# Optimization experiments

Measured on AMD Instinct MI355X. Metric: run time of the kernel, lower is better.

## Reference

```python
import jax, jax.numpy as jnp
import numpy as np

N, F, H, EMB, R, E, B = 100000, 128, 128, 64, 3, 1600000, 1024


def rgcn_conv(x, edge_src, edge_dst, edge_type, W_rel, W_root, b):
    # PyG RGCNConv with aggr='mean': out_i = x_i @ W_root + b + sum_r mean_{j in N_r(i)} x_j @ W_r
    n = x.shape[0]
    r = W_rel.shape[0]
    xr = jnp.einsum('nf,rfh->rnh', x, W_rel)            # [R,N,H] per-relation transform
    msg = xr[edge_type, edge_src]                       # [E,H] gather per edge
    seg = edge_type.astype(jnp.int32) * n + edge_dst    # fused (rel, dst) segment id
    agg = jax.ops.segment_sum(msg, seg, num_segments=r * n).reshape(r, n, -1)
    cnt = jax.ops.segment_sum(jnp.ones((msg.shape[0],), msg.dtype), seg, num_segments=r * n)
    cnt = cnt.reshape(r, n, 1)
    agg = agg / jnp.maximum(cnt, 1.0)
    return agg.sum(0) + x @ W_root + b


def setup_inputs() -> dict:
    key = jax.random.key(0)
    ks = jax.random.split(key, 16)
    s = 0.05
    return {
        'x': jax.random.normal(ks[0], (N, F), jnp.float32),
        'edge_src': jax.random.randint(ks[1], (E,), 0, N, jnp.int32),
        'edge_dst': jax.random.randint(ks[2], (E,), 0, N, jnp.int32),
        'edge_type': jax.random.randint(ks[3], (E,), 0, R, jnp.int32),
        'edge_attr': jax.random.uniform(ks[4], (E, 2), jnp.float32),
        'nest': jax.random.randint(ks[5], (B,), 0, N, jnp.int32),
        'food': jax.random.randint(ks[6], (B,), 0, N, jnp.int32),
        'W_rel1': jax.random.normal(ks[7], (R, F, H), jnp.float32) * s,
        'W_root1': jax.random.normal(ks[8], (F, H), jnp.float32) * s,
        'b1': jnp.zeros((H,), jnp.float32),
        'W_rel2': jax.random.normal(ks[9], (R, H, EMB), jnp.float32) * s,
        'W_root2': jax.random.normal(ks[10], (H, EMB), jnp.float32) * s,
        'b2': jnp.zeros((EMB,), jnp.float32),
        'fc_W': jax.random.normal(ks[11], (2 * EMB, H), jnp.float32) * s,
        'fc_b': jnp.zeros((H,), jnp.float32),
    }


def reference(x, edge_src, edge_dst, edge_type, edge_attr, nest, food,
              W_rel1, W_root1, b1, W_rel2, W_root2, b2, fc_W, fc_b):
    # distance binning (computed in the original forward but unused downstream)
    d = edge_attr[:, 0]
    dmin, dmax = d.min(), d.max()
    bin_size = (dmax - dmin) / 3
    binned = jnp.clip(jnp.floor((d - dmin) / bin_size), 0, 2)
    del binned

    h1 = jax.nn.relu(rgcn_conv(x, edge_src, edge_dst, edge_type, W_rel1, W_root1, b1))
    node = rgcn_conv(h1, edge_src, edge_dst, edge_type, W_rel2, W_root2, b2)  # [N,EMB]
    pair = jnp.concatenate([node[nest], node[food]], axis=-1)  # [B, 2*EMB]
    return jnp.tanh(pair @ fc_W + fc_b)
```

## Files before the change

kernel.cpp:

```cpp
#include <hip/hip_runtime.h>
#include <stdint.h>

typedef unsigned short u16;
typedef __attribute__((ext_vector_type(8))) short short8;
typedef __attribute__((ext_vector_type(4))) float f32x4;
typedef __attribute__((ext_vector_type(2))) float f32x2;
typedef __attribute__((ext_vector_type(4))) unsigned int u32x4;

#define N_NODES 100000
#define RREL    3
#define NEDGE   1600000
#define NPAIR   1024
#define NSEG    (RREL * N_NODES)

#define EPB   4096
#define NBLK  ((NEDGE + EPB - 1) / EPB)
#define DPB   512
#define NBIN  ((N_NODES + DPB - 1) / DPB)
#define LSEG  (DPB * RREL)
#define CAP   12288

#define PREP_TW   384
#define PREP_CAST (N_NODES * 128 / 4 / 256)

__device__ __forceinline__ float bflo(unsigned int u) {
    union { unsigned int u; float f; } c; c.u = u << 16; return c.f;
}
__device__ __forceinline__ float bfhi(unsigned int u) {
    union { unsigned int u; float f; } c; c.u = u & 0xffff0000u; return c.f;
}
__device__ __forceinline__ u16 f2bf(float f) {
    union { float f; unsigned int u; } c; c.f = f;
    unsigned int u = c.u;
    u += 0x7fffu + ((u >> 16) & 1u);
    return (u16)(u >> 16);
}

__device__ __forceinline__ void async_copy16(const u16* g, u16* l) {
    __builtin_amdgcn_global_load_lds(
        (const __attribute__((address_space(1))) unsigned int*)g,
        (__attribute__((address_space(3))) unsigned int*)l,
        16, 0, 0);
}

__global__ __launch_bounds__(256) void prep_kernel(const int* __restrict__ es,
                                                   const int* __restrict__ ed,
                                                   const int* __restrict__ et,
                                                   int* __restrict__ gpos,
                                                   unsigned int* __restrict__ binned,
                                                   const float* __restrict__ x,
                                                   u16* __restrict__ xb,
                                                   const float* __restrict__ Wrel1,
                                                   const float* __restrict__ Wroot1,
                                                   const float* __restrict__ Wrel2,
                                                   const float* __restrict__ Wroot2,
                                                   u16* __restrict__ Wt1,
                                                   u16* __restrict__ Wt2) {
    __shared__ int h[NBIN];
    __shared__ int base[NBIN];
    int b = blockIdx.x, t = threadIdx.x;
    if (b < NBLK) {
        for (int i = t; i < NBIN; i += 256) h[i] = 0;
        __syncthreads();
        int e0 = b * EPB;
        int e1 = e0 + EPB; if (e1 > NEDGE) e1 = NEDGE;
        for (int i = e0 + t; i < e1; i += 256)
            atomicAdd(&h[ed[i] >> 9], 1);
        __syncthreads();
        for (int i = t; i < NBIN; i += 256) {
            int c = h[i];
            base[i] = c ? atomicAdd(&gpos[i], c) : 0;
            h[i] = 0;
        }
        __syncthreads();
        for (int i = e0 + t; i < e1; i += 256) {
            int d = ed[i];
            int bin = d >> 9;
            unsigned int pk = ((unsigned int)es[i] << 11) | (unsigned int)((d & 511) * 3 + et[i]);
            int off = atomicAdd(&h[bin], 1);
            binned[(size_t)bin * CAP + base[bin] + off] = pk;
        }
    } else if (b < NBLK + PREP_TW) {
        int idx = (b - NBLK) * 256 + t;
        if (idx < 128 * 512) {
            int n = idx >> 9, k = idx & 511;
            float v = (k < 384) ? Wrel1[(size_t)k * 128 + n] : Wroot1[(size_t)(k - 384) * 128 + n];
            Wt1[idx] = f2bf(v);
        } else {
            int j = idx - 128 * 512;
            if (j < 256 * 128) {
                int n = j >> 7, k = j & 127;
                float v = (n < 192) ? Wrel2[((size_t)(n >> 6) * 128 + k) * 64 + (n & 63)]
                                    : Wroot2[(size_t)k * 64 + (n - 192)];
                Wt2[j] = f2bf(v);
            }
        }
    } else {
        int i = (b - NBLK - PREP_TW) * 256 + t;
        f32x4 v = __builtin_nontemporal_load(&((const f32x4*)x)[i]);
        uint2 o;
        o.x = ((unsigned int)f2bf(v.y) << 16) | (unsigned int)f2bf(v.x);
        o.y = ((unsigned int)f2bf(v.w) << 16) | (unsigned int)f2bf(v.z);
        ((uint2*)xb)[i] = o;
    }
}

__global__ __launch_bounds__(256) void p4_finalize(const unsigned int* __restrict__ binned,
                                                   const int* __restrict__ gpos,
                                                   int* __restrict__ seg_start,
                                                   int* __restrict__ cnt,
                                                   int* __restrict__ sorted_src) {
    __shared__ int h[LSEG];
    __shared__ int cur[LSEG];
    __shared__ int wtot4[4];
    int t = threadIdx.x, bin = blockIdx.x;
    for (int i = t; i < LSEG; i += 256) h[i] = 0;
    __syncthreads();
    int eb = bin * CAP;
    int ee = eb + gpos[bin];
    for (int i = eb + t; i < ee; i += 256)
        atomicAdd(&h[binned[i] & 2047u], 1);
    __syncthreads();
    int i6 = t * 6;
    int s = 0;
    #pragma unroll
    for (int i = 0; i < 6; ++i) s += h[i6 + i];
    int lane = t & 63, wv = t >> 6;
    int incl = s;
    #pragma unroll
    for (int d = 1; d < 64; d <<= 1) { int v = __shfl_up(incl, d); if (lane >= d) incl += v; }
    if (lane == 63) wtot4[wv] = incl;
    __syncthreads();
    int wpre = 0;
    #pragma unroll
    for (int i = 0; i < 4; ++i) if (i < wv) wpre += wtot4[i];
    int run = wpre + incl - s;
    int segbase = bin * LSEG;
    #pragma unroll
    for (int i = 0; i < 6; ++i) {
        int ls = i6 + i;
        int c = h[ls];
        int seg = segbase + ls;
        if (seg < NSEG) { seg_start[seg] = eb + run; cnt[seg] = c; }
        cur[ls] = run;
        run += c;
    }
    __syncthreads();
    for (int i = eb + t; i < ee; i += 256) {
        unsigned int u = binned[i];
        int ls = (int)(u & 2047u);
        int p = atomicAdd(&cur[ls], 1);
        sorted_src[eb + p] = (int)(u >> 11);
    }
}

__global__ __launch_bounds__(512, 8) void fused_l1(const uint4* __restrict__ X4,
                                                   const u16* __restrict__ xb,
                                                   const int* __restrict__ seg_start,
                                                   const int* __restrict__ cnt,
                                                   const int* __restrict__ sorted_src,
                                                   const u16* __restrict__ Wt1,
                                                   const float* __restrict__ b1,
                                                   u16* __restrict__ h1) {
    __shared__ __align__(16) u16 Aagg[32 * 392];
    __shared__ __align__(16) u16 Aroot[32 * 32];
    __shared__ __align__(16) u16 Bs[128 * 32];
    const int t = threadIdx.x;
    const int w = t >> 6, l = t & 63;
    const int q4 = l >> 4, ql = l & 15;
    const int qid = w * 4 + q4;
    const int bm  = blockIdx.x * 32;
    const int bm3 = blockIdx.x * 96;
    const int shbase = q4 * 16;

    int cArr[3], stArr[3];
    #pragma unroll
    for (int sp = 0; sp < 3; ++sp) {
        int wid = bm3 + sp * 32 + qid;
        cArr[sp]  = cnt[wid];
        stArr[sp] = seg_start[wid];
    }
    #pragma unroll 1
    for (int sp = 0; sp < 3; ++sp) {
        int seg_local = sp * 32 + qid;
        int c  = cArr[sp];
        int st = stArr[sp];

        float a0 = 0.f, a1 = 0.f, a2 = 0.f, a3 = 0.f,
              a4 = 0.f, a5 = 0.f, a6 = 0.f, a7 = 0.f;

        for (int base = 0; base < c; base += 16) {
            int rem = c - base;
            int ii  = (ql < rem) ? ql : (rem - 1);
            int idxv = sorted_src[st + base + ii];
            int lim = (rem < 16) ? rem : 16;
            for (int j = 0; j < lim; j += 4) {
                int e1 = j + 1, e2 = j + 2, e3 = j + 3;
                float w1 = (e1 < lim) ? 1.f : 0.f;
                float w2 = (e2 < lim) ? 1.f : 0.f;
                float w3 = (e3 < lim) ? 1.f : 0.f;
                int s0 = __shfl(idxv, shbase + j);
                int s1 = __shfl(idxv, shbase + ((e1 < lim) ? e1 : 0));
                int s2 = __shfl(idxv, shbase + ((e2 < lim) ? e2 : 0));
                int s3 = __shfl(idxv, shbase + ((e3 < lim) ? e3 : 0));
                uint4 v0 = X4[(size_t)s0 * 16 + ql];
                uint4 v1 = X4[(size_t)s1 * 16 + ql];
                uint4 v2 = X4[(size_t)s2 * 16 + ql];
                uint4 v3 = X4[(size_t)s3 * 16 + ql];
                a0 += bflo(v0.x);               a1 += bfhi(v0.x);
                a2 += bflo(v0.y);               a3 += bfhi(v0.y);
                a4 += bflo(v0.z);               a5 += bfhi(v0.z);
                a6 += bflo(v0.w);               a7 += bfhi(v0.w);
                a0 = fmaf(w1, bflo(v1.x), a0);  a1 = fmaf(w1, bfhi(v1.x), a1);
                a2 = fmaf(w1, bflo(v1.y), a2);  a3 = fmaf(w1, bfhi(v1.y), a3);
                a4 = fmaf(w1, bflo(v1.z), a4);  a5 = fmaf(w1, bfhi(v1.z), a5);
                a6 = fmaf(w1, bflo(v1.w), a6);  a7 = fmaf(w1, bfhi(v1.w), a7);
                a0 = fmaf(w2, bflo(v2.x), a0);  a1 = fmaf(w2, bfhi(v2.x), a1);
                a2 = fmaf(w2, bflo(v2.y), a2);  a3 = fmaf(w2, bfhi(v2.y), a3);
                a4 = fmaf(w2, bflo(v2.z), a4);  a5 = fmaf(w2, bfhi(v2.z), a5);
                a6 = fmaf(w2, bflo(v2.w), a6);  a7 = fmaf(w2, bfhi(v2.w), a7);
                a0 = fmaf(w3, bflo(v3.x), a0);  a1 = fmaf(w3, bfhi(v3.x), a1);
                a2 = fmaf(w3, bflo(v3.y), a2);  a3 = fmaf(w3, bfhi(v3.y), a3);
                a4 = fmaf(w3, bflo(v3.z), a4);  a5 = fmaf(w3, bfhi(v3.z), a5);
                a6 = fmaf(w3, bflo(v3.w), a6);  a7 = fmaf(w3, bfhi(v3.w), a7);
            }
        }
        float sc = 1.0f / (float)(c > 0 ? c : 1);
        u32x4 o;
        o.x = ((unsigned int)f2bf(a1 * sc) << 16) | (unsigned int)f2bf(a0 * sc);
        o.y = ((unsigned int)f2bf(a3 * sc) << 16) | (unsigned int)f2bf(a2 * sc);
        o.z = ((unsigned int)f2bf(a5 * sc) << 16) | (unsigned int)f2bf(a4 * sc);
        o.w = ((unsigned int)f2bf(a7 * sc) << 16) | (unsigned int)f2bf(a6 * sc);
        int n_loc = seg_local / 3;
        int rel   = seg_local - n_loc * 3;
        *(u32x4*)&Aagg[n_loc * 392 + rel * 128 + ql * 8] = o;
    }
    __syncthreads();

    const int wm = w >> 2, wn = w & 3;
    const int q = l >> 4, lm = l & 15;
    f32x4 acc[2] = {};
    const int br  = t >> 2;
    const int bc4 = (t & 3) * 8;

    for (int kt = 0; kt < 16; ++kt) {
        const int k0 = kt * 32;
        __syncthreads();
        async_copy16(Wt1 + (size_t)br * 512 + k0 + bc4, &Bs[br * 32 + bc4]);
        if (kt >= 12 && w < 2) {
            async_copy16(xb + (size_t)(bm + br) * 128 + (k0 - 384) + bc4, &Aroot[br * 32 + bc4]);
        }
        __syncthreads();
        short8 fa;
        if (kt < 12) fa = *(const short8*)&Aagg[(wm * 16 + lm) * 392 + k0 + q * 8];
        else         fa = *(const short8*)&Aroot[(wm * 16 + lm) * 32 + q * 8];
        #pragma unroll
        for (int ni = 0; ni < 2; ++ni) {
            short8 fb = *(const short8*)&Bs[(wn * 32 + ni * 16 + lm) * 32 + q * 8];
            acc[ni] = __builtin_amdgcn_mfma_f32_16x16x32_bf16(fa, fb, acc[ni], 0, 0, 0);
        }
    }
    #pragma unroll
    for (int ni = 0; ni < 2; ++ni) {
        int gc = wn * 32 + ni * 16 + lm;
        float bv = b1[gc];
        #pragma unroll
        for (int rg = 0; rg < 4; ++rg) {
            int gr = bm + wm * 16 + q * 4 + rg;
            float v = fmaxf(acc[ni][rg] + bv, 0.0f);
            h1[(size_t)gr * 128 + gc] = f2bf(v);
        }
    }
}

__global__ __launch_bounds__(256) void seg_pair(const u16* __restrict__ P,
                                                const int* __restrict__ seg_start,
                                                const int* __restrict__ cnt,
                                                const int* __restrict__ sorted_src,
                                                const float* __restrict__ node,
                                                const int* __restrict__ nest,
                                                const int* __restrict__ food,
                                                float* __restrict__ pairbuf) {
    int lane = threadIdx.x & 63;
    int q4 = lane >> 4, ql = lane & 15;
    int e  = ql >> 3;
    int fl = ql & 7;
    int slot = ((blockIdx.x * 256 + threadIdx.x) >> 6) * 4 + q4;
    int p = slot >> 1, side = slot & 1;
    int dst = side ? food[p] : nest[p];
    if ((unsigned)dst >= (unsigned)N_NODES) dst = 0;
    int shbase = q4 * 16;

    int c0 = cnt[dst * 3 + 0], c1 = cnt[dst * 3 + 1], c2 = cnt[dst * 3 + 2];
    int st = seg_start[dst * 3 + 0];
    int c01 = c0 + c1, tot = c01 + c2;
    float r0 = c0 ? 1.0f / (float)c0 : 0.0f;
    float r1 = c1 ? 1.0f / (float)c1 : 0.0f;
    float r2 = c2 ? 1.0f / (float)c2 : 0.0f;

    const f32x4* np = (const f32x4*)(node + (size_t)dst * 64 + fl * 8);
    f32x4 z0 = *np;
    f32x4 z1 = *(np + 1);

    f32x2 d0 = {0.f,0.f}, d1 = {0.f,0.f}, d2 = {0.f,0.f}, d3 = {0.f,0.f};

    for (int base = 0; base < tot; base += 16) {
        int rem = tot - base;
        int ii  = (ql < rem) ? ql : 0;
        int idxv = sorted_src[st + base + ii];
        int lim = (rem < 16) ? rem : 16;

        uint4 v[8];
        #pragma unroll
        for (int k = 0; k < 8; ++k) {
            int jj = 2 * k + e;
            int sel = (jj < lim) ? jj : 0;
            int s = __shfl(idxv, shbase + sel);
            int ge = base + sel;
            int rel = (ge >= c0) + (ge >= c01);
            v[k] = *(const uint4*)(P + (size_t)s * 192 + rel * 64 + fl * 8);
        }
        #pragma unroll
        for (int k = 0; k < 8; ++k) {
            int jj = 2 * k + e;
            int ge = base + jj;
            float wr = (jj < lim) ? ((ge < c0) ? r0 : ((ge < c01) ? r1 : r2)) : 0.0f;
            f32x2 wv = {wr, wr};
            d0 += wv * (f32x2){bflo(v[k].x), bfhi(v[k].x)};
            d1 += wv * (f32x2){bflo(v[k].y), bfhi(v[k].y)};
            d2 += wv * (f32x2){bflo(v[k].z), bfhi(v[k].z)};
            d3 += wv * (f32x2){bflo(v[k].w), bfhi(v[k].w)};
        }
    }
    d0.x += __shfl_xor(d0.x, 8); d0.y += __shfl_xor(d0.y, 8);
    d1.x += __shfl_xor(d1.x, 8); d1.y += __shfl_xor(d1.y, 8);
    d2.x += __shfl_xor(d2.x, 8); d2.y += __shfl_xor(d2.y, 8);
    d3.x += __shfl_xor(d3.x, 8); d3.y += __shfl_xor(d3.y, 8);
    if (e == 0) {
        f32x4 o0 = {z0.x + d0.x, z0.y + d0.y, z0.z + d1.x, z0.w + d1.y};
        f32x4 o1 = {z1.x + d2.x, z1.y + d2.y, z1.z + d3.x, z1.w + d3.y};
        f32x4* op = (f32x4*)(pairbuf + (size_t)p * 128 + side * 64 + fl * 8);
        *op       = o0;
        *(op + 1) = o1;
    }
}

template <int BM, int BN, int KTOT, int KLO, bool RELU, int OMODE>
__global__ __launch_bounds__(256) void gemm_fused(const u16* __restrict__ Alo,
                                                  const u16* __restrict__ Ahi,
                                                  const u16* __restrict__ Wt,
                                                  const float* __restrict__ bias,
                                                  void* __restrict__ OutV,
                                                  float* __restrict__ Out2) {
    constexpr int M = N_NODES;
    constexpr int BK = 32;
    __shared__ __align__(16) u16 As[BM * BK];
    __shared__ __align__(16) u16 Bs[BN * BK];
    const int t = threadIdx.x;
    const int w = t >> 6, l = t & 63;
    const int bm = blockIdx.x * BM;
    constexpr int WN  = BN / 64;
    constexpr int WM  = 4 / WN;
    constexpr int WTM = BM / WM;
    constexpr int WTN = 64;
    constexpr int MI = WTM / 16, NI = WTN / 16;
    const int wm = w / WN, wn = w % WN;
    const int q = l >> 4, lm = l & 15;

    f32x4 acc[MI][NI] = {};

    const int ar = t >> 2;
    const int ac = (t & 3) * 8;

    int gr0 = bm + ar;       if (gr0 >= M) gr0 = M - 1;
    int gr1 = bm + 64 + ar;  if (gr1 >= M) gr1 = M - 1;

    for (int kt = 0; kt < KTOT / BK; ++kt) {
        const int k0 = kt * BK;
        const u16* base; int stride, kk;
        if (k0 < KLO) { base = Alo; stride = KLO == KTOT ? KTOT : 384; kk = k0; }
        else          { base = Ahi; stride = 128; kk = k0 - KLO; }
        __syncthreads();
        async_copy16(base + (size_t)gr0 * stride + kk + ac, &As[ar * BK + ac]);
        if (BM == 128)
            async_copy16(base + (size_t)gr1 * stride + kk + ac, &As[(64 + ar) * BK + ac]);
        #pragma unroll
        for (int i = 0; i < BN / 64; ++i)
            async_copy16(Wt + (size_t)(i * 64 + ar) * KTOT + k0 + ac,
                         &Bs[(i * 64 + ar) * BK + ac]);
        __syncthreads();
        short8 fa[MI], fb[NI];
        #pragma unroll
        for (int mi = 0; mi < MI; ++mi)
            fa[mi] = *(const short8*)&As[(wm * WTM + mi * 16 + lm) * BK + q * 8];
        #pragma unroll
        for (int ni = 0; ni < NI; ++ni)
            fb[ni] = *(const short8*)&Bs[(wn * WTN + ni * 16 + lm) * BK + q * 8];
        #pragma unroll
        for (int mi = 0; mi < MI; ++mi)
            #pragma unroll
            for (int ni = 0; ni < NI; ++ni)
                acc[mi][ni] = __builtin_amdgcn_mfma_f32_16x16x32_bf16(
                    fa[mi], fb[ni], acc[mi][ni], 0, 0, 0);
    }
    #pragma unroll
    for (int mi = 0; mi < MI; ++mi) {
        #pragma unroll
        for (int ni = 0; ni < NI; ++ni) {
            int gc = wn * WTN + ni * 16 + lm;
            float bv;
            if (OMODE == 2) bv = (gc >= 192) ? bias[gc - 192] : 0.0f;
            else            bv = bias[gc];
            #pragma unroll
            for (int rg = 0; rg < 4; ++rg) {
                int gr = bm + wm * WTM + mi * 16 + q * 4 + rg;
                if (gr < M) {
                    float v = acc[mi][ni][rg] + bv;
                    if (RELU) v = fmaxf(v, 0.0f);
                    if (OMODE == 0)      ((u16*)OutV)[(size_t)gr * BN + gc] = f2bf(v);
                    else if (OMODE == 1) ((float*)OutV)[(size_t)gr * BN + gc] = v;
                    else {
                        if (gc < 192) ((u16*)OutV)[(size_t)gr * 192 + gc] = f2bf(v);
                        else          Out2[(size_t)gr * 64 + (gc - 192)] = v;
                    }
                }
            }
        }
    }
}

__global__ __launch_bounds__(128) void pair_mlp(const float* __restrict__ pairbuf,
                                                const float* __restrict__ fcW,
                                                const float* __restrict__ fcb,
                                                float* __restrict__ out) {
    int p = blockIdx.x;
    int t = threadIdx.x;
    __shared__ float pv[128];
    pv[t] = pairbuf[(size_t)p * 128 + t];
    __syncthreads();
    float s = fcb[t];
    #pragma unroll 4
    for (int k = 0; k < 128; ++k)
        s += pv[k] * fcW[k * 128 + t];
    out[(size_t)p * 128 + t] = tanhf(s);
}

extern "C" void kernel_launch(void* const* d_in, const int* in_sizes, int n_in,
                              void* d_out, int out_size, void* d_ws, size_t ws_size,
                              hipStream_t stream) {
    const float* x    = (const float*)d_in[0];
    const int* esrc   = (const int*)d_in[1];
    const int* edst   = (const int*)d_in[2];
    const int* etyp   = (const int*)d_in[3];
    const int* nest   = (const int*)d_in[5];
    const int* food   = (const int*)d_in[6];
    const float* Wrel1  = (const float*)d_in[7];
    const float* Wroot1 = (const float*)d_in[8];
    const float* b1     = (const float*)d_in[9];
    const float* Wrel2  = (const float*)d_in[10];
    const float* Wroot2 = (const float*)d_in[11];
    const float* b2     = (const float*)d_in[12];
    const float* fcW    = (const float*)d_in[13];
    const float* fcb    = (const float*)d_in[14];
    float* out = (float*)d_out;

    char* ws = (char*)d_ws;
    size_t off = 0;
    auto alloc_b = [&](size_t bytes) -> void* {
        void* p = ws + off;
        off += (bytes + 255) & ~(size_t)255;
        return p;
    };
    int* gpos        = (int*)alloc_b((size_t)NBIN * 4);
    unsigned int* bn = (unsigned int*)alloc_b((size_t)NBIN * CAP * 4);
    int* seg_start   = (int*)alloc_b((size_t)NSEG * 4);
    int* cnt         = (int*)alloc_b((size_t)NSEG * 4);
    int* sorted_src  = (int*)alloc_b((size_t)NBIN * CAP * 4);
    u16* Wt1         = (u16*)alloc_b((size_t)128 * 512 * 2);
    u16* Wt2         = (u16*)alloc_b((size_t)256 * 128 * 2);
    u16* xb          = (u16*)alloc_b((size_t)N_NODES * 128 * 2);
    u16* P           = (u16*)alloc_b((size_t)N_NODES * 192 * 2);
    u16* h1          = (u16*)alloc_b((size_t)N_NODES * 128 * 2);
    float* node      = (float*)alloc_b((size_t)N_NODES * 64 * 4);
    float* pairbuf   = (float*)alloc_b((size_t)NPAIR * 128 * 4);

    hipMemsetAsync(gpos, 0, (size_t)NBIN * 4, stream);

    prep_kernel<<<NBLK + PREP_TW + PREP_CAST, 256, 0, stream>>>(
        esrc, edst, etyp, gpos, bn, x, xb, Wrel1, Wroot1, Wrel2, Wroot2, Wt1, Wt2);

    p4_finalize<<<NBIN, 256, 0, stream>>>(bn, gpos, seg_start, cnt, sorted_src);

    const int gemmBlocks2 = (N_NODES + 63) / 64;

    fused_l1<<<N_NODES / 32, 512, 0, stream>>>(
        (const uint4*)xb, xb, seg_start, cnt, sorted_src, Wt1, b1, h1);

    gemm_fused<64, 256, 128, 128, false, 2><<<gemmBlocks2, 256, 0, stream>>>(
        h1, h1, Wt2, b2, P, node);
    seg_pair<<<(NPAIR * 2) / 16, 256, 0, stream>>>(
        P, seg_start, cnt, sorted_src, node, nest, food, pairbuf);

    pair_mlp<<<NPAIR, 128, 0, stream>>>(pairbuf, fcW, fcb, out);
}
```

Baseline: 321.6 us.

## Restrict layer-1 and layer-2 compute to nodes reachable from query pairs

```diff
diff --git a/kernel.cpp b/kernel.cpp
--- a/kernel.cpp
+++ b/kernel.cpp
@@ -154,6 +154,37 @@
     }
 }
 
+__global__ __launch_bounds__(256) void mark_nodes(const int* __restrict__ nest,
+                                                  const int* __restrict__ food,
+                                                  const int* __restrict__ seg_start,
+                                                  const int* __restrict__ cnt,
+                                                  const int* __restrict__ sorted_src,
+                                                  int* __restrict__ flag) {
+    int slot = blockIdx.x * 256 + threadIdx.x;
+    if (slot >= NPAIR * 2) return;
+    int p = slot >> 1, side = slot & 1;
+    int dst = side ? food[p] : nest[p];
+    if ((unsigned)dst >= (unsigned)N_NODES) dst = 0;
+    flag[dst] = 1;
+    int tot = cnt[dst * 3] + cnt[dst * 3 + 1] + cnt[dst * 3 + 2];
+    int st = seg_start[dst * 3];
+    for (int i = 0; i < tot; ++i)
+        flag[sorted_src[st + i]] = 1;
+}
+
+__global__ __launch_bounds__(256) void compact_nodes(const int* __restrict__ flag,
+                                                     int* __restrict__ ncnt,
+                                                     int* __restrict__ list,
+                                                     int* __restrict__ map) {
+    int n = blockIdx.x * 256 + threadIdx.x;
+    if (n >= N_NODES) return;
+    if (flag[n]) {
+        int idx = atomicAdd(ncnt, 1);
+        list[idx] = n;
+        map[n] = idx;
+    }
+}
+
 __global__ __launch_bounds__(512, 8) void fused_l1(const uint4* __restrict__ X4,
                                                    const u16* __restrict__ xb,
                                                    const int* __restrict__ seg_start,
@@ -161,7 +192,12 @@
                                                    const int* __restrict__ sorted_src,
                                                    const u16* __restrict__ Wt1,
                                                    const float* __restrict__ b1,
-                                                   u16* __restrict__ h1) {
+                                                   const int* __restrict__ list,
+                                                   const int* __restrict__ ncnt,
+                                                   u16* __restrict__ h1c) {
+    const int nc = *ncnt;
+    const int bm  = blockIdx.x * 32;
+    if (bm >= nc) return;
     __shared__ __align__(16) u16 Aagg[32 * 392];
     __shared__ __align__(16) u16 Aroot[32 * 32];
     __shared__ __align__(16) u16 Bs[128 * 32];
@@ -169,16 +205,16 @@
     const int w = t >> 6, l = t & 63;
     const int q4 = l >> 4, ql = l & 15;
     const int qid = w * 4 + q4;
-    const int bm  = blockIdx.x * 32;
-    const int bm3 = blockIdx.x * 96;
     const int shbase = q4 * 16;
 
     int cArr[3], stArr[3];
     #pragma unroll
     for (int sp = 0; sp < 3; ++sp) {
-        int wid = bm3 + sp * 32 + qid;
-        cArr[sp]  = cnt[wid];
-        stArr[sp] = seg_start[wid];
+        int seg_local = sp * 32 + qid;
+        int n_loc = seg_local / 3, rel = seg_local - n_loc * 3;
+        int nid = list[bm + n_loc];
+        cArr[sp]  = cnt[nid * 3 + rel];
+        stArr[sp] = seg_start[nid * 3 + rel];
     }
     #pragma unroll 1
     for (int sp = 0; sp < 3; ++sp) {
@@ -248,7 +284,7 @@
         __syncthreads();
         async_copy16(Wt1 + (size_t)br * 512 + k0 + bc4, &Bs[br * 32 + bc4]);
         if (kt >= 12 && w < 2) {
-            async_copy16(xb + (size_t)(bm + br) * 128 + (k0 - 384) + bc4, &Aroot[br * 32 + bc4]);
+            async_copy16(xb + (size_t)list[bm + br] * 128 + (k0 - 384) + bc4, &Aroot[br * 32 + bc4]);
         }
         __syncthreads();
         short8 fa;
@@ -268,16 +304,81 @@
         for (int rg = 0; rg < 4; ++rg) {
             int gr = bm + wm * 16 + q * 4 + rg;
             float v = fmaxf(acc[ni][rg] + bv, 0.0f);
-            h1[(size_t)gr * 128 + gc] = f2bf(v);
-        }
-    }
-}
-
-__global__ __launch_bounds__(256) void seg_pair(const u16* __restrict__ P,
+            h1c[(size_t)gr * 128 + gc] = f2bf(v);
+        }
+    }
+}
+
+__global__ __launch_bounds__(256) void gemm2_c(const u16* __restrict__ h1c,
+                                               const u16* __restrict__ Wt2,
+                                               const float* __restrict__ b2,
+                                               const int* __restrict__ ncnt,
+                                               u16* __restrict__ Pc,
+                                               float* __restrict__ nodec) {
+    const int nc = *ncnt;
+    const int bm = blockIdx.x * 64;
+    if (bm >= nc) return;
+    __shared__ __align__(16) u16 As[64 * 32];
+    __shared__ __align__(16) u16 Bs[256 * 32];
+    const int t = threadIdx.x;
+    const int w = t >> 6, l = t & 63;
+    const int wn = w;
+    const int q = l >> 4, lm = l & 15;
+
+    f32x4 acc[4][4] = {};
+    const int ar = t >> 2;
+    const int ac = (t & 3) * 8;
+
+    int gr0 = bm + ar; if (gr0 >= nc) gr0 = nc - 1;
+
+    for (int kt = 0; kt < 4; ++kt) {
+        const int k0 = kt * 32;
+        __syncthreads();
+        async_copy16(h1c + (size_t)gr0 * 128 + k0 + ac, &As[ar * 32 + ac]);
+        #pragma unroll
+        for (int i = 0; i < 4; ++i)
+            async_copy16(Wt2 + (size_t)(i * 64 + ar) * 128 + k0 + ac,
+                         &Bs[(i * 64 + ar) * 32 + ac]);
+        __syncthreads();
+        short8 fa[4], fb[4];
+        #pragma unroll
+        for (int mi = 0; mi < 4; ++mi)
+            fa[mi] = *(const short8*)&As[(mi * 16 + lm) * 32 + q * 8];
+        #pragma unroll
+        for (int ni = 0; ni < 4; ++ni)
+            fb[ni] = *(const short8*)&Bs[(wn * 64 + ni * 16 + lm) * 32 + q * 8];
+        #pragma unroll
+        for (int mi = 0; mi < 4; ++mi)
+            #pragma unroll
+            for (int ni = 0; ni < 4; ++ni)
+                acc[mi][ni] = __builtin_amdgcn_mfma_f32_16x16x32_bf16(
+                    fa[mi], fb[ni], acc[mi][ni], 0, 0, 0);
+    }
+    #pragma unroll
+    for (int mi = 0; mi < 4; ++mi) {
+        #pragma unroll
+        for (int ni = 0; ni < 4; ++ni) {
+            int gc = wn * 64 + ni * 16 + lm;
+            float bv = (gc >= 192) ? b2[gc - 192] : 0.0f;
+            #pragma unroll
+            for (int rg = 0; rg < 4; ++rg) {
+                int gr = bm + mi * 16 + q * 4 + rg;
+                if (gr < nc) {
+                    float v = acc[mi][ni][rg] + bv;
+                    if (gc < 192) Pc[(size_t)gr * 192 + gc] = f2bf(v);
+                    else          nodec[(size_t)gr * 64 + (gc - 192)] = v;
+                }
+            }
+        }
+    }
+}
+
+__global__ __launch_bounds__(256) void seg_pair(const u16* __restrict__ Pc,
                                                 const int* __restrict__ seg_start,
                                                 const int* __restrict__ cnt,
                                                 const int* __restrict__ sorted_src,
-                                                const float* __restrict__ node,
+                                                const float* __restrict__ nodec,
+                                                const int* __restrict__ map,
                                                 const int* __restrict__ nest,
                                                 const int* __restrict__ food,
                                                 float* __restrict__ pairbuf) {
@@ -298,7 +399,7 @@
     float r1 = c1 ? 1.0f / (float)c1 : 0.0f;
     float r2 = c2 ? 1.0f / (float)c2 : 0.0f;
 
-    const f32x4* np = (const f32x4*)(node + (size_t)dst * 64 + fl * 8);
+    const f32x4* np = (const f32x4*)(nodec + (size_t)map[dst] * 64 + fl * 8);
     f32x4 z0 = *np;
     f32x4 z1 = *(np + 1);
 
@@ -318,7 +419,7 @@
             int s = __shfl(idxv, shbase + sel);
             int ge = base + sel;
             int rel = (ge >= c0) + (ge >= c01);
-            v[k] = *(const uint4*)(P + (size_t)s * 192 + rel * 64 + fl * 8);
+            v[k] = *(const uint4*)(Pc + (size_t)map[s] * 192 + rel * 64 + fl * 8);
         }
         #pragma unroll
         for (int k = 0; k < 8; ++k) {
@@ -342,90 +443,6 @@
         f32x4* op = (f32x4*)(pairbuf + (size_t)p * 128 + side * 64 + fl * 8);
         *op       = o0;
         *(op + 1) = o1;
-    }
-}
-
-template <int BM, int BN, int KTOT, int KLO, bool RELU, int OMODE>
-__global__ __launch_bounds__(256) void gemm_fused(const u16* __restrict__ Alo,
-                                                  const u16* __restrict__ Ahi,
-                                                  const u16* __restrict__ Wt,
-                                                  const float* __restrict__ bias,
-                                                  void* __restrict__ OutV,
-                                                  float* __restrict__ Out2) {
-    constexpr int M = N_NODES;
-    constexpr int BK = 32;
-    __shared__ __align__(16) u16 As[BM * BK];
-    __shared__ __align__(16) u16 Bs[BN * BK];
-    const int t = threadIdx.x;
-    const int w = t >> 6, l = t & 63;
-    const int bm = blockIdx.x * BM;
-    constexpr int WN  = BN / 64;
-    constexpr int WM  = 4 / WN;
-    constexpr int WTM = BM / WM;
-    constexpr int WTN = 64;
-    constexpr int MI = WTM / 16, NI = WTN / 16;
-    const int wm = w / WN, wn = w % WN;
-    const int q = l >> 4, lm = l & 15;
-
-    f32x4 acc[MI][NI] = {};
-
-    const int ar = t >> 2;
-    const int ac = (t & 3) * 8;
-
-    int gr0 = bm + ar;       if (gr0 >= M) gr0 = M - 1;
-    int gr1 = bm + 64 + ar;  if (gr1 >= M) gr1 = M - 1;
-
-    for (int kt = 0; kt < KTOT / BK; ++kt) {
-        const int k0 = kt * BK;
-        const u16* base; int stride, kk;
-        if (k0 < KLO) { base = Alo; stride = KLO == KTOT ? KTOT : 384; kk = k0; }
-        else          { base = Ahi; stride = 128; kk = k0 - KLO; }
-        __syncthreads();
-        async_copy16(base + (size_t)gr0 * stride + kk + ac, &As[ar * BK + ac]);
-        if (BM == 128)
-            async_copy16(base + (size_t)gr1 * stride + kk + ac, &As[(64 + ar) * BK + ac]);
-        #pragma unroll
-        for (int i = 0; i < BN / 64; ++i)
-            async_copy16(Wt + (size_t)(i * 64 + ar) * KTOT + k0 + ac,
-                         &Bs[(i * 64 + ar) * BK + ac]);
-        __syncthreads();
-        short8 fa[MI], fb[NI];
-        #pragma unroll
-        for (int mi = 0; mi < MI; ++mi)
-            fa[mi] = *(const short8*)&As[(wm * WTM + mi * 16 + lm) * BK + q * 8];
-        #pragma unroll
-        for (int ni = 0; ni < NI; ++ni)
-            fb[ni] = *(const short8*)&Bs[(wn * WTN + ni * 16 + lm) * BK + q * 8];
-        #pragma unroll
-        for (int mi = 0; mi < MI; ++mi)
-            #pragma unroll
-            for (int ni = 0; ni < NI; ++ni)
-                acc[mi][ni] = __builtin_amdgcn_mfma_f32_16x16x32_bf16(
-                    fa[mi], fb[ni], acc[mi][ni], 0, 0, 0);
-    }
-    #pragma unroll
-    for (int mi = 0; mi < MI; ++mi) {
-        #pragma unroll
-        for (int ni = 0; ni < NI; ++ni) {
-            int gc = wn * WTN + ni * 16 + lm;
-            float bv;
-            if (OMODE == 2) bv = (gc >= 192) ? bias[gc - 192] : 0.0f;
-            else            bv = bias[gc];
-            #pragma unroll
-            for (int rg = 0; rg < 4; ++rg) {
-                int gr = bm + wm * WTM + mi * 16 + q * 4 + rg;
-                if (gr < M) {
-                    float v = acc[mi][ni][rg] + bv;
-                    if (RELU) v = fmaxf(v, 0.0f);
-                    if (OMODE == 0)      ((u16*)OutV)[(size_t)gr * BN + gc] = f2bf(v);
-                    else if (OMODE == 1) ((float*)OutV)[(size_t)gr * BN + gc] = v;
-                    else {
-                        if (gc < 192) ((u16*)OutV)[(size_t)gr * 192 + gc] = f2bf(v);
-                        else          Out2[(size_t)gr * 64 + (gc - 192)] = v;
-                    }
-                }
-            }
-        }
     }
 }
 
@@ -479,27 +496,34 @@
     u16* Wt1         = (u16*)alloc_b((size_t)128 * 512 * 2);
     u16* Wt2         = (u16*)alloc_b((size_t)256 * 128 * 2);
     u16* xb          = (u16*)alloc_b((size_t)N_NODES * 128 * 2);
-    u16* P           = (u16*)alloc_b((size_t)N_NODES * 192 * 2);
-    u16* h1          = (u16*)alloc_b((size_t)N_NODES * 128 * 2);
-    float* node      = (float*)alloc_b((size_t)N_NODES * 64 * 4);
+    u16* Pc          = (u16*)alloc_b((size_t)N_NODES * 192 * 2);
+    u16* h1c         = (u16*)alloc_b((size_t)N_NODES * 128 * 2);
+    float* nodec     = (float*)alloc_b((size_t)N_NODES * 64 * 4);
     float* pairbuf   = (float*)alloc_b((size_t)NPAIR * 128 * 4);
+    int* ncnt        = (int*)alloc_b(4);
+    int* flag        = (int*)alloc_b((size_t)N_NODES * 4);
+    int* list        = (int*)alloc_b((size_t)N_NODES * 4);
+    size_t zspan     = (size_t)((char*)(list + N_NODES) - (char*)ncnt);
+    int* map         = (int*)alloc_b((size_t)N_NODES * 4);
 
     hipMemsetAsync(gpos, 0, (size_t)NBIN * 4, stream);
+    hipMemsetAsync(ncnt, 0, zspan, stream);
 
     prep_kernel<<<NBLK + PREP_TW + PREP_CAST, 256, 0, stream>>>(
         esrc, edst, etyp, gpos, bn, x, xb, Wrel1, Wroot1, Wrel2, Wroot2, Wt1, Wt2);
 
     p4_finalize<<<NBIN, 256, 0, stream>>>(bn, gpos, seg_start, cnt, sorted_src);
 
-    const int gemmBlocks2 = (N_NODES + 63) / 64;
+    mark_nodes<<<(NPAIR * 2 + 255) / 256, 256, 0, stream>>>(
+        nest, food, seg_start, cnt, sorted_src, flag);
+    compact_nodes<<<(N_NODES + 255) / 256, 256, 0, stream>>>(flag, ncnt, list, map);
 
     fused_l1<<<N_NODES / 32, 512, 0, stream>>>(
-        (const uint4*)xb, xb, seg_start, cnt, sorted_src, Wt1, b1, h1);
-
-    gemm_fused<64, 256, 128, 128, false, 2><<<gemmBlocks2, 256, 0, stream>>>(
-        h1, h1, Wt2, b2, P, node);
+        (const uint4*)xb, xb, seg_start, cnt, sorted_src, Wt1, b1, list, ncnt, h1c);
+
+    gemm2_c<<<(N_NODES + 63) / 64, 256, 0, stream>>>(h1c, Wt2, b2, ncnt, Pc, nodec);
     seg_pair<<<(NPAIR * 2) / 16, 256, 0, stream>>>(
-        P, seg_start, cnt, sorted_src, node, nest, food, pairbuf);
+        Pc, seg_start, cnt, sorted_src, nodec, map, nest, food, pairbuf);
 
     pair_mlp<<<NPAIR, 128, 0, stream>>>(pairbuf, fcW, fcb, out);
 }
```

Result: faster. 271.5 us (-15.6%).
